# Performance work log

Hardware: AMD Instinct MI355X
Metric: run time of the kernel (lower is better)

The kernel has to match this reference:

```python
import jax, jax.numpy as jnp
import numpy as np

B, S, E = 2, 2048, 1024
H, D = 16, 64          # num_heads, head_dim
FF = 4096              # ff_dim = 4*E
EPS = 1e-5


def _layer_norm(x, g, b):
    mu = jnp.mean(x, axis=-1, keepdims=True)
    var = jnp.mean(jnp.square(x - mu), axis=-1, keepdims=True)
    return (x - mu) * jax.lax.rsqrt(var + EPS) * g + b


def setup_inputs() -> dict:
    key = jax.random.key(0)
    ks = jax.random.split(key, 9)
    s = lambda fan_in: 1.0 / np.sqrt(fan_in)
    return {
        "x": jax.random.normal(ks[0], (B, S, E), dtype=jnp.float32),
        "w_qkv": jax.random.uniform(ks[1], (3 * E, E), jnp.float32, -s(E), s(E)),
        "b_qkv": jnp.zeros((3 * E,), jnp.float32),
        "w_out": jax.random.uniform(ks[2], (E, E), jnp.float32, -s(E), s(E)),
        "b_out": jnp.zeros((E,), jnp.float32),
        "g1": jnp.ones((E,), jnp.float32),
        "beta1": jnp.zeros((E,), jnp.float32),
        "w_fc1": jax.random.uniform(ks[3], (FF, E), jnp.float32, -s(E), s(E)),
        "b_fc1": jnp.zeros((FF,), jnp.float32),
        "w_fc2": jax.random.uniform(ks[4], (E, FF), jnp.float32, -s(FF), s(FF)),
        "b_fc2": jnp.zeros((E,), jnp.float32),
        "g2": jnp.ones((E,), jnp.float32),
        "beta2": jnp.zeros((E,), jnp.float32),
    }


def reference(x, w_qkv, b_qkv, w_out, b_out, g1, beta1, w_fc1, b_fc1, w_fc2, b_fc2, g2, beta2):
    scale = 1.0 / np.sqrt(D)
    # QKV projection: [B,S,3E] -> [3,B,H,S,D]
    qkv = (x @ w_qkv.T + b_qkv).reshape(B, S, 3, H, D).transpose(2, 0, 3, 1, 4)
    q, k, v = qkv[0], qkv[1], qkv[2]
    attn = jax.nn.softmax(jnp.einsum('bhqd,bhkd->bhqk', q, k) * scale, axis=-1)
    out = jnp.einsum('bhqk,bhkd->bhqd', attn, v)          # [B,H,S,D]
    out = out.transpose(0, 2, 1, 3).reshape(B, S, E)
    attn_out = out @ w_out.T + b_out
    x1 = _layer_norm(x + attn_out, g1, beta1)
    h = jax.nn.gelu(x1 @ w_fc1.T + b_fc1, approximate=False)  # torch GELU = exact erf
    ff_out = h @ w_fc2.T + b_fc2
    return _layer_norm(x1 + ff_out, g2, beta2)
```

## Files before the change

### kernel.cpp

```cpp
#include <hip/hip_runtime.h>
#include <hip/hip_bf16.h>
#include <math.h>
#include <type_traits>

typedef __hip_bfloat16 bf16;
using short8  = __attribute__((ext_vector_type(8))) short;
using short4v = __attribute__((ext_vector_type(4))) short;
using f32x4   = __attribute__((ext_vector_type(4))) float;

#define TS 2048
#define TH 16
#define TD 64
#define TE 1024
#define T2E 2048

__device__ __forceinline__ void gload16(void* lds, const void* g) {
    __builtin_amdgcn_global_load_lds(
        (__attribute__((address_space(1))) void*)g,
        (__attribute__((address_space(3))) void*)lds, 16, 0, 0);
}

__device__ __forceinline__ uint32_t pktrunc(float a, float b) {
    return (__builtin_bit_cast(uint32_t, a) >> 16) |
           (__builtin_bit_cast(uint32_t, b) & 0xFFFF0000u);
}

__global__ __launch_bounds__(256) void f2b_multi(
    const float* __restrict__ s0, bf16* __restrict__ d0,
    const float* __restrict__ s1, bf16* __restrict__ d1,
    const float* __restrict__ s2, bf16* __restrict__ d2,
    const float* __restrict__ s3, bf16* __restrict__ d3,
    const float* __restrict__ s4, bf16* __restrict__ d4)
{
    int blk = blockIdx.x;
    const float* s; bf16* d; int base;
    if (blk < 2048)      { s = s0; d = d0; base = 0; }
    else if (blk < 3584) { s = s1; d = d1; base = 2048; }
    else if (blk < 4096) { s = s2; d = d2; base = 3584; }
    else if (blk < 6144) { s = s3; d = d3; base = 4096; }
    else                 { s = s4; d = d4; base = 6144; }
    size_t i = ((size_t)(blk - base) * 256 + threadIdx.x) * 8;
    float4 a = *(const float4*)&s[i];
    float4 b = *(const float4*)&s[i + 4];
    bf16 t[8];
    t[0] = __float2bfloat16(a.x); t[1] = __float2bfloat16(a.y);
    t[2] = __float2bfloat16(a.z); t[3] = __float2bfloat16(a.w);
    t[4] = __float2bfloat16(b.x); t[5] = __float2bfloat16(b.y);
    t[6] = __float2bfloat16(b.z); t[7] = __float2bfloat16(b.w);
    *(uint4*)&d[i] = *(uint4*)t;
}

template <typename TC, bool GELU, bool QS, bool WVT, int BN>
__global__ __launch_bounds__(512, 2) void gemm256(
    const bf16* __restrict__ A, const bf16* __restrict__ Bw,
    const float* __restrict__ bias, TC* __restrict__ C,
    bf16* __restrict__ vTout, int M, int N, int K, int kLen, int Cstride)
{
    constexpr int NB = BN / 64;
    constexpr int NI = BN / 64;
    constexpr int WN = BN / 4;
    __shared__ bf16 As[2][256 * 64];
    __shared__ bf16 Bs[2][BN * 64];

    const int t    = threadIdx.x;
    const int lane = t & 63;
    const int wv   = t >> 6;
    const int wr   = wv >> 2;
    const int wc   = wv & 3;
    const int lr   = lane & 15;
    const int lq   = lane >> 4;

    const int gx  = gridDim.x, gxy = gridDim.x * gridDim.y;
    const int nwg = gxy * gridDim.z;
    const int id  = blockIdx.x + gx * blockIdx.y + gxy * blockIdx.z;
    const int sid = (id & 7) * (nwg >> 3) + (id >> 3);
    const int zIdx  = sid / gxy;
    const int rem   = sid - zIdx * gxy;
    const int tm    = rem / gx;
    const int mBase = tm * 256;
    const int nBase = (rem - tm * gx) * BN;
    const int kOff  = zIdx * kLen;

    const int sr = t >> 3;
    const int sc = (((t & 7) ^ ((t >> 3) & 7)) * 8);
    const int NT = kLen >> 6;

    const bf16* aPt = A  + (size_t)(mBase + sr) * K + sc;
    const bf16* bPt = Bw + (size_t)(nBase + sr) * K + sc;

    f32x4 acc[8][NI];
    #pragma unroll
    for (int mi = 0; mi < 8; mi++)
        #pragma unroll
        for (int ni = 0; ni < NI; ni++)
            acc[mi][ni] = (f32x4){0.f, 0.f, 0.f, 0.f};

    auto stage = [&](int b, int k0) {
        #pragma unroll
        for (int i = 0; i < 4; i++)
            gload16(&As[b][i * 4096 + wv * 512],
                    aPt + (size_t)(i * 64) * K + k0);
        #pragma unroll
        for (int i = 0; i < NB; i++)
            gload16(&Bs[b][i * 4096 + wv * 512],
                    bPt + (size_t)(i * 64) * K + k0);
    };

    stage(0, kOff);
    for (int kt = 0; kt < NT; ++kt) {
        const int cur = kt & 1;
        if (kt + 1 < NT) {
            stage(cur ^ 1, kOff + (kt + 1) * 64);
            if constexpr (BN == 256)
                asm volatile("s_waitcnt vmcnt(8)" ::: "memory");
            else if constexpr (BN == 192)
                asm volatile("s_waitcnt vmcnt(7)" ::: "memory");
            else
                asm volatile("s_waitcnt vmcnt(6)" ::: "memory");
        } else {
            asm volatile("s_waitcnt vmcnt(0)" ::: "memory");
        }
        __builtin_amdgcn_s_barrier();
        asm volatile("" ::: "memory");

        short8 bfr[NI][2];
        #pragma unroll
        for (int ni = 0; ni < NI; ni++)
            #pragma unroll
            for (int ks = 0; ks < 2; ks++) {
                int row = wc * WN + ni * 16 + lr;
                int col = (ks * 32 + lq * 8) ^ ((lr & 7) * 8);
                bfr[ni][ks] = *(const short8*)&Bs[cur][row * 64 + col];
            }
        #pragma unroll
        for (int mi = 0; mi < 8; mi++) {
            int row = wr * 128 + mi * 16 + lr;
            int c0 = (lq * 8) ^ ((lr & 7) * 8);
            int c1 = (32 + lq * 8) ^ ((lr & 7) * 8);
            short8 a0 = *(const short8*)&As[cur][row * 64 + c0];
            short8 a1 = *(const short8*)&As[cur][row * 64 + c1];
            #pragma unroll
            for (int ni = 0; ni < NI; ni++) {
                acc[mi][ni] = __builtin_amdgcn_mfma_f32_16x16x32_bf16(
                    a0, bfr[ni][0], acc[mi][ni], 0, 0, 0);
                acc[mi][ni] = __builtin_amdgcn_mfma_f32_16x16x32_bf16(
                    a1, bfr[ni][1], acc[mi][ni], 0, 0, 0);
            }
        }
        asm volatile("s_waitcnt lgkmcnt(0)" ::: "memory");
        __builtin_amdgcn_s_barrier();
    }

    const size_t cOff = (size_t)zIdx * M * Cstride;
    #pragma unroll
    for (int mi = 0; mi < 8; mi++) {
        #pragma unroll
        for (int ni = 0; ni < NI; ni++) {
            int cc = nBase + wc * WN + ni * 16 + lr;
            float bv = (zIdx == 0) ? bias[cc] : 0.f;
            int r0 = mBase + wr * 128 + mi * 16 + lq * 4;
            bool vpath = false;
            if constexpr (WVT) {
                if (cc >= 2 * TE) {
                    vpath = true;
                    int d  = cc - 2 * TE;
                    int s0 = r0 & (TS - 1);
                    int bb = r0 >> 11;
                    int pos = (s0 & ~31) | (((s0 >> 2) & 3) << 3)
                            | (((s0 >> 4) & 1) << 2);
                    bf16 ob[4];
                    #pragma unroll
                    for (int i = 0; i < 4; i++)
                        ob[i] = __float2bfloat16(acc[mi][ni][i] + bv);
                    *(uint2*)&vTout[((size_t)(bb * TH + (d >> 6)) * TD + (d & 63))
                                    * TS + pos] = *(uint2*)ob;
                }
            }
            if (!vpath) {
                #pragma unroll
                for (int i = 0; i < 4; i++) {
                    float v = acc[mi][ni][i] + bv;
                    if constexpr (GELU)
                        v = 0.5f * v * (1.0f + erff(v * 0.70710678118f));
                    if constexpr (QS)
                        if (cc < TE) v *= 0.180336880111f;
                    if constexpr (std::is_same_v<TC, bf16>)
                        C[cOff + (size_t)(r0 + i) * Cstride + cc] = __float2bfloat16(v);
                    else
                        C[cOff + (size_t)(r0 + i) * Cstride + cc] = v;
                }
            }
        }
    }
}

__global__ __launch_bounds__(512, 2) void gemm128n(
    const bf16* __restrict__ A, const bf16* __restrict__ Bw,
    const float* __restrict__ bias, float* __restrict__ C,
    int M, int N, int K, int kLen)
{
    __shared__ bf16 As[3][128 * 64];
    __shared__ bf16 Bs[3][256 * 64];

    const int t    = threadIdx.x;
    const int lane = t & 63;
    const int wv   = t >> 6;
    const int wr   = wv >> 2;
    const int wc   = wv & 3;
    const int lr   = lane & 15;
    const int lq   = lane >> 4;

    const int gx  = gridDim.x, gxy = gridDim.x * gridDim.y;
    const int nwg = gxy * gridDim.z;
    const int id  = blockIdx.x + gx * blockIdx.y + gxy * blockIdx.z;
    const int sid = (id & 7) * (nwg >> 3) + (id >> 3);
    const int zIdx  = sid / gxy;
    const int rem   = sid - zIdx * gxy;
    const int tm    = rem / gx;
    const int mBase = tm * 128;
    const int nBase = (rem - tm * gx) * 256;
    const int kOff  = zIdx * kLen;

    const int sr = t >> 3;
    const int sc = (((t & 7) ^ ((t >> 3) & 7)) * 8);

    const bf16* aPt = A  + (size_t)(mBase + sr) * K + sc;
    const bf16* bPt = Bw + (size_t)(nBase + sr) * K + sc;

    f32x4 acc[4][4];
    #pragma unroll
    for (int mi = 0; mi < 4; mi++)
        #pragma unroll
        for (int ni = 0; ni < 4; ni++)
            acc[mi][ni] = (f32x4){0.f, 0.f, 0.f, 0.f};

    auto stage = [&](int b, int k0) {
        #pragma unroll
        for (int i = 0; i < 2; i++)
            gload16(&As[b][i * 4096 + wv * 512],
                    aPt + (size_t)(i * 64) * K + k0);
        #pragma unroll
        for (int i = 0; i < 4; i++)
            gload16(&Bs[b][i * 4096 + wv * 512],
                    bPt + (size_t)(i * 64) * K + k0);
    };

    const int NT = kLen >> 6;
    stage(0, kOff);
    stage(1, kOff + 64);
    int cur = 0;
    for (int kt = 0; kt < NT; ++kt) {
        if (kt + 2 < NT) {
            int nb = cur + 2; if (nb >= 3) nb -= 3;
            stage(nb, kOff + (kt + 2) * 64);
            asm volatile("s_waitcnt vmcnt(12)" ::: "memory");
        } else if (kt + 1 < NT) {
            asm volatile("s_waitcnt vmcnt(6)" ::: "memory");
        } else {
            asm volatile("s_waitcnt vmcnt(0)" ::: "memory");
        }
        __builtin_amdgcn_s_barrier();
        asm volatile("" ::: "memory");

        short8 af[4][2], bfr[4][2];
        #pragma unroll
        for (int mi = 0; mi < 4; mi++)
            #pragma unroll
            for (int ks = 0; ks < 2; ks++) {
                int row = wr * 64 + mi * 16 + lr;
                int col = (ks * 32 + lq * 8) ^ ((lr & 7) * 8);
                af[mi][ks] = *(const short8*)&As[cur][row * 64 + col];
            }
        #pragma unroll
        for (int ni = 0; ni < 4; ni++)
            #pragma unroll
            for (int ks = 0; ks < 2; ks++) {
                int row = wc * 64 + ni * 16 + lr;
                int col = (ks * 32 + lq * 8) ^ ((lr & 7) * 8);
                bfr[ni][ks] = *(const short8*)&Bs[cur][row * 64 + col];
            }
        #pragma unroll
        for (int mi = 0; mi < 4; mi++)
            #pragma unroll
            for (int ni = 0; ni < 4; ni++) {
                acc[mi][ni] = __builtin_amdgcn_mfma_f32_16x16x32_bf16(
                    af[mi][0], bfr[ni][0], acc[mi][ni], 0, 0, 0);
                acc[mi][ni] = __builtin_amdgcn_mfma_f32_16x16x32_bf16(
                    af[mi][1], bfr[ni][1], acc[mi][ni], 0, 0, 0);
            }
        asm volatile("s_waitcnt lgkmcnt(0)" ::: "memory");
        __builtin_amdgcn_s_barrier();
        cur += 1; if (cur >= 3) cur = 0;
    }

    const size_t cOff = (size_t)zIdx * M * N;
    #pragma unroll
    for (int mi = 0; mi < 4; mi++) {
        #pragma unroll
        for (int ni = 0; ni < 4; ni++) {
            int cc = nBase + wc * 64 + ni * 16 + lr;
            float bv = (zIdx == 0) ? bias[cc] : 0.f;
            int r0 = mBase + wr * 64 + mi * 16 + lq * 4;
            #pragma unroll
            for (int i = 0; i < 4; i++)
                C[cOff + (size_t)(r0 + i) * N + cc] = acc[mi][ni][i] + bv;
        }
    }
}

__global__ __launch_bounds__(256, 2) void attn_flash(
    const bf16* __restrict__ qkv, const bf16* __restrict__ vT,
    bf16* __restrict__ attnO)
{
    __shared__ bf16 Ks[128 * 72];
    __shared__ bf16 Vt[64 * 136];

    const int t    = threadIdx.x;
    const int lane = t & 63;
    const int wv   = t >> 6;
    const int c    = lane & 15;
    const int u    = lane >> 4;
    const int bid  = blockIdx.x;
    const int bh   = (bid & 7) * 4 + ((bid >> 3) & 3);
    const int qt   = bid >> 5;
    const int h = bh & 15, b = bh >> 4;
    const size_t tokBase = (size_t)b * TS;
    const int qrow0 = qt * 128 + wv * 32 + c;

    short8 qf[2][2];
    #pragma unroll
    for (int d = 0; d < 2; d++)
        #pragma unroll
        for (int kc = 0; kc < 2; kc++)
            qf[d][kc] = *(const short8*)&qkv[(tokBase + qrow0 + d * 16) * T2E
                                             + h * TD + kc * 32 + u * 8];

    f32x4 oacc[2][4];
    #pragma unroll
    for (int d = 0; d < 2; d++)
        #pragma unroll
        for (int di = 0; di < 4; di++) oacc[d][di] = (f32x4){0.f, 0.f, 0.f, 0.f};
    float lsum[2] = {0.f, 0.f};

    for (int it = 0; it < 16; it++) {
        const int kb0 = it * 128;
        __syncthreads();

        #pragma unroll
        for (int i = 0; i < 4; i++) {
            int l = t + i * 256;
            int r = l >> 3, ch = (l & 7) * 8;
            *(uint4*)&Ks[r * 72 + ch] =
                *(const uint4*)&qkv[(tokBase + kb0 + r) * T2E + TE + h * TD + ch];
        }
        #pragma unroll
        for (int i = 0; i < 4; i++) {
            int c0 = t + i * 256;
            int vd = c0 >> 4, vcc = (c0 & 15) * 8;
            *(uint4*)&Vt[vd * 136 + vcc] =
                *(const uint4*)&vT[((size_t)bh * TD + vd) * TS + kb0 + vcc];
        }
        __syncthreads();

        f32x4 sacc[2][8];
        #pragma unroll
        for (int kc = 0; kc < 2; kc++) {
            #pragma unroll
            for (int kb = 0; kb < 8; kb++) {
                short8 kf = *(const short8*)&Ks[(kb * 16 + c) * 72 + kc * 32 + u * 8];
                #pragma unroll
                for (int d = 0; d < 2; d++)
                    sacc[d][kb] = __builtin_amdgcn_mfma_f32_16x16x32_bf16(
                        kf, qf[d][kc],
                        kc == 0 ? (f32x4){0.f, 0.f, 0.f, 0.f} : sacc[d][kb],
                        0, 0, 0);
            }
        }

        #pragma unroll
        for (int p = 0; p < 4; p++) {
            union { uint32_t dd[2]; short4v s; } pb0[2], pb1[2];
            #pragma unroll
            for (int d = 0; d < 2; d++) {
                float a0 = exp2f(sacc[d][2*p][0]);
                float a1 = exp2f(sacc[d][2*p][1]);
                float a2 = exp2f(sacc[d][2*p][2]);
                float a3 = exp2f(sacc[d][2*p][3]);
                float b0 = exp2f(sacc[d][2*p+1][0]);
                float b1 = exp2f(sacc[d][2*p+1][1]);
                float b2 = exp2f(sacc[d][2*p+1][2]);
                float b3 = exp2f(sacc[d][2*p+1][3]);
                lsum[d] += (a0 + a1) + (a2 + a3) + (b0 + b1) + (b2 + b3);
                pb0[d].dd[0] = pktrunc(a0, a1); pb0[d].dd[1] = pktrunc(a2, a3);
                pb1[d].dd[0] = pktrunc(b0, b1); pb1[d].dd[1] = pktrunc(b2, b3);
            }
            #pragma unroll
            for (int di = 0; di < 4; di++) {
                short8 vv = *(const short8*)&Vt[(di * 16 + c) * 136 + p * 32 + u * 8];
                short4v lo = __builtin_shufflevector(vv, vv, 0, 1, 2, 3);
                short4v hi = __builtin_shufflevector(vv, vv, 4, 5, 6, 7);
                #pragma unroll
                for (int d = 0; d < 2; d++) {
                    oacc[d][di] = __builtin_amdgcn_mfma_f32_16x16x16bf16_1k(
                        lo, pb0[d].s, oacc[d][di], 0, 0, 0);
                    oacc[d][di] = __builtin_amdgcn_mfma_f32_16x16x16bf16_1k(
                        hi, pb1[d].s, oacc[d][di], 0, 0, 0);
                }
            }
        }
    }

    #pragma unroll
    for (int d = 0; d < 2; d++) {
        float ls = lsum[d];
        ls += __shfl_xor(ls, 16, 64);
        ls += __shfl_xor(ls, 32, 64);
        const float inv = 1.0f / ls;
        #pragma unroll
        for (int di = 0; di < 4; di++) {
            bf16 ob[4];
            #pragma unroll
            for (int rg = 0; rg < 4; rg++)
                ob[rg] = __float2bfloat16(oacc[d][di][rg] * inv);
            *(uint2*)&attnO[(tokBase + qrow0 + d * 16) * TE + h * TD
                            + di * 16 + u * 4] = *(uint2*)ob;
        }
    }
}

__global__ __launch_bounds__(256) void add_ln3(
    const float* __restrict__ a, const float* __restrict__ p0,
    const float* __restrict__ p1, const float* __restrict__ g,
    const float* __restrict__ beta, float* __restrict__ out,
    bf16* __restrict__ outb)
{
    __shared__ float r1[256], r2[256];
    const int t = threadIdx.x;
    const size_t row = (size_t)blockIdx.x * TE;

    float4 va = *(const float4*)&a[row + t * 4];
    float4 v0 = *(const float4*)&p0[row + t * 4];
    float4 v1 = *(const float4*)&p1[row + t * 4];
    float v[4] = {va.x + v0.x + v1.x, va.y + v0.y + v1.y,
                  va.z + v0.z + v1.z, va.w + v0.w + v1.w};
    float s = 0.f, s2 = 0.f;
    #pragma unroll
    for (int i = 0; i < 4; i++) { s += v[i]; s2 += v[i] * v[i]; }
    r1[t] = s; r2[t] = s2;
    __syncthreads();
    for (int off = 128; off > 0; off >>= 1) {
        if (t < off) { r1[t] += r1[t + off]; r2[t] += r2[t + off]; }
        __syncthreads();
    }
    const float mu  = r1[0] * (1.f / 1024.f);
    const float var = r2[0] * (1.f / 1024.f) - mu * mu;
    const float rs  = rsqrtf(var + 1e-5f);
    float4 vg  = *(const float4*)&g[t * 4];
    float4 vbt = *(const float4*)&beta[t * 4];
    float o[4];
    o[0] = (v[0] - mu) * rs * vg.x + vbt.x;
    o[1] = (v[1] - mu) * rs * vg.y + vbt.y;
    o[2] = (v[2] - mu) * rs * vg.z + vbt.z;
    o[3] = (v[3] - mu) * rs * vg.w + vbt.w;
    *(float4*)&out[row + t * 4] = *(float4*)o;
    if (outb) {
        bf16 ob[4];
        #pragma unroll
        for (int i = 0; i < 4; i++) ob[i] = __float2bfloat16(o[i]);
        *(uint2*)&outb[row + t * 4] = *(uint2*)ob;
    }
}

extern "C" void kernel_launch(void* const* d_in, const int* in_sizes, int n_in,
                              void* d_out, int out_size, void* d_ws, size_t ws_size,
                              hipStream_t stream)
{
    const float* x     = (const float*)d_in[0];
    const float* w_qkv = (const float*)d_in[1];
    const float* b_qkv = (const float*)d_in[2];
    const float* w_out = (const float*)d_in[3];
    const float* b_out = (const float*)d_in[4];
    const float* g1    = (const float*)d_in[5];
    const float* beta1 = (const float*)d_in[6];
    const float* w_fc1 = (const float*)d_in[7];
    const float* b_fc1 = (const float*)d_in[8];
    const float* w_fc2 = (const float*)d_in[9];
    const float* b_fc2 = (const float*)d_in[10];
    const float* g2    = (const float*)d_in[11];
    const float* beta2 = (const float*)d_in[12];
    float* out = (float*)d_out;

    char* wsb   = (char*)d_ws;
    bf16*  qk    = (bf16*)(wsb);
    bf16*  vT    = (bf16*)(wsb + 16777216);
    bf16*  xb    = (bf16*)(wsb + 25165824);
    float* y     = (float*)(wsb);
    float* ff    = (float*)(wsb);
    bf16*  attnO = (bf16*)(wsb + 33554432);
    bf16*  x1b   = (bf16*)(wsb + 33554432);
    bf16*  wfc1b = (bf16*)(wsb + 41943040);
    bf16*  woutb = (bf16*)(wsb + 50331648);
    bf16*  wqkvb = (bf16*)(wsb + 52428800);
    float* x1    = (float*)(wsb + 67108864);
    bf16*  hbuf  = (bf16*)(wsb + 83886080);
    bf16*  wfc2b = (bf16*)(wsb + 117440512);

    const int M = 2 * TS;
    const size_t PART = (size_t)M * TE;
    dim3 blk(256), blk8(512);

    f2b_multi<<<dim3(8192), blk, 0, stream>>>(
        x, xb, w_qkv, wqkvb, w_out, woutb, w_fc1, wfc1b, w_fc2, wfc2b);

    gemm256<bf16, false, true, true, 192><<<dim3(16, 16, 1), blk8, 0, stream>>>(
        xb, wqkvb, b_qkv, qk, vT, M, 3072, TE, TE, T2E);
    attn_flash<<<dim3(512), blk, 0, stream>>>(qk, vT, attnO);
    gemm128n<<<dim3(4, 32, 2), blk8, 0, stream>>>(
        attnO, woutb, b_out, y, M, TE, TE, TE / 2);
    add_ln3<<<dim3(M), blk, 0, stream>>>(x, y, y + PART, g1, beta1, x1, x1b);
    gemm256<bf16, true, false, false, 256><<<dim3(16, 16, 1), blk8, 0, stream>>>(
        x1b, wfc1b, b_fc1, hbuf, nullptr, M, 4096, TE, TE, 4096);
    gemm128n<<<dim3(4, 32, 2), blk8, 0, stream>>>(
        hbuf, wfc2b, b_fc2, ff, M, TE, 4096, 2048);
    add_ln3<<<dim3(M), blk, 0, stream>>>(x1, ff, ff + PART, g2, beta2, out, nullptr);
}
```

Before: 361.2 us.

## Register-prefetch next K/V tile and use 16x16x32 MFMA for PV

```diff
diff --git a/kernel.cpp b/kernel.cpp
--- a/kernel.cpp
+++ b/kernel.cpp
@@ -342,25 +342,33 @@
         for (int di = 0; di < 4; di++) oacc[d][di] = (f32x4){0.f, 0.f, 0.f, 0.f};
     float lsum[2] = {0.f, 0.f};
 
+    const int kr  = t >> 3, kch = (t & 7) * 8;
+    const int vd  = t >> 4, vcc = (t & 15) * 8;
+    const bf16* kbase = &qkv[(tokBase + kr) * T2E + TE + h * TD + kch];
+    const bf16* vbase = &vT[((size_t)bh * TD + vd) * TS + vcc];
+
+    uint4 kreg[4], vreg[4];
+    auto loadKV = [&](int kb0) {
+        #pragma unroll
+        for (int i = 0; i < 4; i++)
+            kreg[i] = *(const uint4*)&kbase[(size_t)(kb0 + i * 32) * T2E];
+        #pragma unroll
+        for (int i = 0; i < 4; i++)
+            vreg[i] = *(const uint4*)&vbase[(size_t)(i * 16) * TS + kb0];
+    };
+
+    loadKV(0);
     for (int it = 0; it < 16; it++) {
-        const int kb0 = it * 128;
         __syncthreads();
-
-        #pragma unroll
-        for (int i = 0; i < 4; i++) {
-            int l = t + i * 256;
-            int r = l >> 3, ch = (l & 7) * 8;
-            *(uint4*)&Ks[r * 72 + ch] =
-                *(const uint4*)&qkv[(tokBase + kb0 + r) * T2E + TE + h * TD + ch];
-        }
-        #pragma unroll
-        for (int i = 0; i < 4; i++) {
-            int c0 = t + i * 256;
-            int vd = c0 >> 4, vcc = (c0 & 15) * 8;
-            *(uint4*)&Vt[vd * 136 + vcc] =
-                *(const uint4*)&vT[((size_t)bh * TD + vd) * TS + kb0 + vcc];
-        }
+        #pragma unroll
+        for (int i = 0; i < 4; i++)
+            *(uint4*)&Ks[(kr + i * 32) * 72 + kch] = kreg[i];
+        #pragma unroll
+        for (int i = 0; i < 4; i++)
+            *(uint4*)&Vt[(vd + i * 16) * 136 + vcc] = vreg[i];
         __syncthreads();
+        if (it + 1 < 16)
+            loadKV((it + 1) * 128);
 
         f32x4 sacc[2][8];
         #pragma unroll
@@ -379,7 +387,7 @@
 
         #pragma unroll
         for (int p = 0; p < 4; p++) {
-            union { uint32_t dd[2]; short4v s; } pb0[2], pb1[2];
+            union { uint32_t dd[4]; short8 s8; } pbc[2];
             #pragma unroll
             for (int d = 0; d < 2; d++) {
                 float a0 = exp2f(sacc[d][2*p][0]);
@@ -391,21 +399,16 @@
                 float b2 = exp2f(sacc[d][2*p+1][2]);
                 float b3 = exp2f(sacc[d][2*p+1][3]);
                 lsum[d] += (a0 + a1) + (a2 + a3) + (b0 + b1) + (b2 + b3);
-                pb0[d].dd[0] = pktrunc(a0, a1); pb0[d].dd[1] = pktrunc(a2, a3);
-                pb1[d].dd[0] = pktrunc(b0, b1); pb1[d].dd[1] = pktrunc(b2, b3);
+                pbc[d].dd[0] = pktrunc(a0, a1); pbc[d].dd[1] = pktrunc(a2, a3);
+                pbc[d].dd[2] = pktrunc(b0, b1); pbc[d].dd[3] = pktrunc(b2, b3);
             }
             #pragma unroll
             for (int di = 0; di < 4; di++) {
                 short8 vv = *(const short8*)&Vt[(di * 16 + c) * 136 + p * 32 + u * 8];
-                short4v lo = __builtin_shufflevector(vv, vv, 0, 1, 2, 3);
-                short4v hi = __builtin_shufflevector(vv, vv, 4, 5, 6, 7);
                 #pragma unroll
-                for (int d = 0; d < 2; d++) {
-                    oacc[d][di] = __builtin_amdgcn_mfma_f32_16x16x16bf16_1k(
-                        lo, pb0[d].s, oacc[d][di], 0, 0, 0);
-                    oacc[d][di] = __builtin_amdgcn_mfma_f32_16x16x16bf16_1k(
-                        hi, pb1[d].s, oacc[d][di], 0, 0, 0);
-                }
+                for (int d = 0; d < 2; d++)
+                    oacc[d][di] = __builtin_amdgcn_mfma_f32_16x16x32_bf16(
+                        vv, pbc[d].s8, oacc[d][di], 0, 0, 0);
             }
         }
     }
```

Result: slower. 381.2 us (+5.6%).
